# Optimization experiments

Hardware: AMD Instinct MI355X
Metric: run time of the kernel (lower is better)

## Reference

```python
import jax, jax.numpy as jnp
import numpy as np

N, H, W = 4, 96, 96
C, G, K = 128, 8, 3
GC = C // G          # group channels = 16
P = K * K            # sampling points per group = 9
PAD = K // 2
OFS = 1.0            # offset_scale
HID = 4 * C          # mlp hidden
EPS = 1e-5           # torch nn.LayerNorm default eps


def _ln(x, g, b):
    m = jnp.mean(x, -1, keepdims=True)
    v = jnp.mean((x - m) ** 2, -1, keepdims=True)
    return (x - m) * jax.lax.rsqrt(v + EPS) * g + b


def _dcnv3_core(x, offset, mask):
    # x: (n,H,W,C) channels-last, offset: (n,H,W,G*P*2), mask: (n,H,W,G,P) softmaxed.
    # Faithful port of dcnv3_core_pytorch (stride=1, dilation=1, zero-pad grid_sample,
    # align_corners=False -> pixel = loc*size - 0.5).
    n = x.shape[0]
    xp = jnp.pad(x, ((0, 0), (PAD, PAD), (PAD, PAD), (0, 0)))
    Hin, Win = H + 2 * PAD, W + 2 * PAD
    L = H * W
    base = (K - 1) // 2 + 0.5
    ref_x = (base + jnp.arange(W, dtype=x.dtype)) / Win  # normalized by padded size
    ref_y = (base + jnp.arange(H, dtype=x.dtype)) / Hin
    k = jnp.arange(K, dtype=x.dtype) - (K - 1) // 2
    dx = jnp.repeat(k, K) / Win  # torch meshgrid('ij'): kernel-x varies slowest
    dy = jnp.tile(k, K) / Hin
    off = offset.reshape(n, H, W, G, P, 2)
    # absolute sampling pixel coords (grid_sample align_corners=False)
    px = (ref_x[None, None, :, None, None] + dx * OFS + off[..., 0] * OFS / Win) * Win - 0.5
    py = (ref_y[None, :, None, None, None] + dy * OFS + off[..., 1] * OFS / Hin) * Hin - 0.5
    # layout (n,G,L,P)
    px = px.transpose(0, 3, 1, 2, 4).reshape(n, G, L, P)
    py = py.transpose(0, 3, 1, 2, 4).reshape(n, G, L, P)
    mk = mask.transpose(0, 3, 1, 2, 4).reshape(n, G, L, P)
    xg = xp.reshape(n, Hin * Win, G, GC).transpose(0, 2, 1, 3)
    x0 = jnp.floor(px); y0 = jnp.floor(py)
    fx = px - x0; fy = py - y0
    x0 = x0.astype(jnp.int32); y0 = y0.astype(jnp.int32)
    x1 = x0 + 1; y1 = y0 + 1
    out = jnp.zeros((n, G, L, GC), x.dtype)
    for yi, xi, w in ((y0, x0, (1 - fy) * (1 - fx)), (y0, x1, (1 - fy) * fx),
                      (y1, x0, fy * (1 - fx)), (y1, x1, fy * fx)):
        valid = (yi >= 0) & (yi < Hin) & (xi >= 0) & (xi < Win)
        idx = jnp.clip(yi, 0, Hin - 1) * Win + jnp.clip(xi, 0, Win - 1)
        v = jnp.take_along_axis(xg, idx.reshape(n, G, L * P, 1), axis=2)
        v = v.reshape(n, G, L, P, GC)
        out = out + jnp.einsum('nglp,nglpc->nglc', jnp.where(valid, w, 0.0) * mk, v)
    return out.transpose(0, 2, 1, 3).reshape(n, H, W, C)


def _dcn(x, w_in, b_in, dw_k, dw_b, dwg, dwb, w_off, b_off, w_msk, b_msk, w_out, b_out):
    n = x.shape[0]
    xproj = x @ w_in + b_in
    x1 = jax.lax.conv_general_dilated(
        x, dw_k, (1, 1), 'SAME',
        dimension_numbers=('NHWC', 'HWIO', 'NHWC'),
        feature_group_count=C) + dw_b
    x1 = jax.nn.gelu(_ln(x1, dwg, dwb), approximate=False)
    offset = x1 @ w_off + b_off
    mask = jax.nn.softmax((x1 @ w_msk + b_msk).reshape(n, H, W, G, P), axis=-1)
    y = _dcnv3_core(xproj, offset, mask)
    return y @ w_out + b_out


def setup_inputs() -> dict:
    key = jax.random.key(0)
    ks = jax.random.split(key, 10)
    rn = lambda k, s, sc: jax.random.normal(k, s, jnp.float32) * sc
    return {
        'x': rn(ks[0], (N, H, W, C), 1.0),
        'ln1g': jnp.ones((C,), jnp.float32), 'ln1b': jnp.zeros((C,), jnp.float32),
        'w_in': rn(ks[1], (C, C), 0.02), 'b_in': jnp.zeros((C,), jnp.float32),
        'dw_k': rn(ks[2], (K, K, 1, C), 0.1), 'dw_b': jnp.zeros((C,), jnp.float32),
        'dwg': jnp.ones((C,), jnp.float32), 'dwb': jnp.zeros((C,), jnp.float32),
        'w_off': rn(ks[3], (C, G * P * 2), 0.01), 'b_off': rn(ks[4], (G * P * 2,), 0.1),
        'w_msk': rn(ks[5], (C, G * P), 0.02), 'b_msk': jnp.zeros((G * P,), jnp.float32),
        'w_out': rn(ks[6], (C, C), 0.02), 'b_out': jnp.zeros((C,), jnp.float32),
        'ln2g': jnp.ones((C,), jnp.float32), 'ln2b': jnp.zeros((C,), jnp.float32),
        'w1': rn(ks[7], (C, HID), 0.02), 'b1': jnp.zeros((HID,), jnp.float32),
        'w2': rn(ks[8], (HID, C), 0.02), 'b2': jnp.zeros((C,), jnp.float32),
    }


def reference(x, ln1g, ln1b, w_in, b_in, dw_k, dw_b, dwg, dwb, w_off, b_off,
              w_msk, b_msk, w_out, b_out, ln2g, ln2b, w1, b1, w2, b2):
    # pre-norm InternImage block: x = x + dcn(LN1(x)); x = x + mlp(LN2(x))
    x = x + _dcn(_ln(x, ln1g, ln1b), w_in, b_in, dw_k, dw_b, dwg, dwb,
                 w_off, b_off, w_msk, b_msk, w_out, b_out)
    h = _ln(x, ln2g, ln2b)
    h = jax.nn.gelu(h @ w1 + b1, approximate=False) @ w2 + b2
    return x + h
```

## Files before the change

### kernel.cpp

```cpp
#include <hip/hip_runtime.h>
#include <hip/hip_bf16.h>
#include <math.h>

using bf16 = __hip_bfloat16;
using bf162 = __hip_bfloat162;

typedef __bf16 bf16x8 __attribute__((ext_vector_type(8)));
typedef float floatx4 __attribute__((ext_vector_type(4)));

constexpr int NB = 4, HH = 96, WW = 96, CC = 128, GG = 8, PP = 9;
constexpr int HW = HH * WW;
constexpr int NPIX = NB * HW;

__device__ __forceinline__ float ld1(const float* p) { return *p; }
__device__ __forceinline__ float ld1(const bf16* p)  { return __bfloat162float(*p); }
__device__ __forceinline__ void st1(float* p, float v) { *p = v; }
__device__ __forceinline__ void st1(bf16* p, float v)  { *p = __float2bfloat16(v); }
__device__ __forceinline__ float b2f(bf16 v) { return __bfloat162float(v); }
__device__ __forceinline__ bf16 f2b(float v) { return __float2bfloat16(v); }
__device__ __forceinline__ float gelu_exact(float v) {
    return 0.5f * v * (1.0f + erff(v * 0.7071067811865475f));
}
__device__ __forceinline__ floatx4 MFMA(bf16x8 a, bf16x8 b, floatx4 c) {
    return __builtin_amdgcn_mfma_f32_16x16x32_bf16(a, b, c, 0, 0, 0);
}

struct PrepArgs {
    const float* src[6];
    bf16* dst[6];
    int K[6], N[6];
    int cum[7];
    const float* b_off; const float* b_msk; float* b_om;
};

__global__ __launch_bounds__(256) void prep_weights(PrepArgs pa, int total)
{
    int t = blockIdx.x * 256 + threadIdx.x;
    if (t >= total) return;
    if (t >= pa.cum[6]) {
        int e = t - pa.cum[6];
        pa.b_om[e] = (e < 144) ? pa.b_off[e] : pa.b_msk[e - 144];
        return;
    }
    int i = 0;
    #pragma unroll
    for (int j = 0; j < 5; ++j) if (t >= pa.cum[j + 1]) i = j + 1;
    int e = t - pa.cum[i];
    int Ki = pa.K[i], Ni = pa.N[i];
    int n = e / Ki, k = e - n * Ki;
    pa.dst[i][e] = f2b(pa.src[i][(size_t)k * Ni + n]);
}

template<typename TI, typename TO>
__global__ __launch_bounds__(256) void ln_kernel(
    const TI* __restrict__ X, const float* __restrict__ g,
    const float* __restrict__ b, TO* __restrict__ out)
{
    int wave = (blockIdx.x * 256 + threadIdx.x) >> 6;
    int lane = threadIdx.x & 63;
    if (wave >= NPIX) return;
    const TI* xp = X + (size_t)wave * 128 + 2 * lane;
    float v0 = ld1(xp), v1 = ld1(xp + 1);
    float s = v0 + v1, q = v0 * v0 + v1 * v1;
    #pragma unroll
    for (int o = 32; o; o >>= 1) { s += __shfl_xor(s, o); q += __shfl_xor(q, o); }
    float mean = s * (1.0f / 128.0f);
    float rstd = rsqrtf(q * (1.0f / 128.0f) - mean * mean + 1e-5f);
    float g0 = g[2 * lane], g1 = g[2 * lane + 1];
    float b0 = b[2 * lane], b1 = b[2 * lane + 1];
    TO* op = out + (size_t)wave * 128 + 2 * lane;
    st1(op,     (v0 - mean) * rstd * g0 + b0);
    st1(op + 1, (v1 - mean) * rstd * g1 + b1);
}

__global__ __launch_bounds__(256) void dwconv_ln_gelu_kernel(
    const bf16* __restrict__ xln, const float* __restrict__ dwk,
    const float* __restrict__ dwb, const float* __restrict__ gam,
    const float* __restrict__ bet, bf16* __restrict__ out)
{
    int wave = (blockIdx.x * 256 + threadIdx.x) >> 6;
    int lane = threadIdx.x & 63;
    if (wave >= NPIX) return;
    int n = wave / HW; int rem = wave % HW;
    int y = rem / WW;  int x = rem % WW;
    const bf162* xp = (const bf162*)xln;
    float a0 = 0.f, a1 = 0.f;
    #pragma unroll
    for (int ky = 0; ky < 3; ++ky) {
        int yy = y + ky - 1;
        if (yy < 0 || yy >= HH) continue;
        #pragma unroll
        for (int kx = 0; kx < 3; ++kx) {
            int xx = x + kx - 1;
            if (xx < 0 || xx >= WW) continue;
            bf162 v = xp[((size_t)(n * HH + yy) * WW + xx) * 64 + lane];
            const float* w = dwk + (ky * 3 + kx) * CC + 2 * lane;
            a0 = fmaf(b2f(v.x), w[0], a0);
            a1 = fmaf(b2f(v.y), w[1], a1);
        }
    }
    a0 += dwb[2 * lane]; a1 += dwb[2 * lane + 1];
    float s = a0 + a1, q = a0 * a0 + a1 * a1;
    #pragma unroll
    for (int o = 32; o; o >>= 1) { s += __shfl_xor(s, o); q += __shfl_xor(q, o); }
    float mean = s * (1.0f / 128.0f);
    float rstd = rsqrtf(q * (1.0f / 128.0f) - mean * mean + 1e-5f);
    float h0 = gelu_exact((a0 - mean) * rstd * gam[2 * lane]     + bet[2 * lane]);
    float h1 = gelu_exact((a1 - mean) * rstd * gam[2 * lane + 1] + bet[2 * lane + 1]);
    bf162 o2; o2.x = f2b(h0); o2.y = f2b(h1);
    ((bf162*)out)[(size_t)wave * 64 + lane] = o2;
}

__global__ __launch_bounds__(256) void dcn_core_kernel(
    const bf16* __restrict__ xproj, const bf16* __restrict__ omr,
    bf16* __restrict__ out)
{
    __shared__ int4   sOff[4][72];
    __shared__ float4 sW[4][72];
    __shared__ float  sRaw[4][72];
    int wv = threadIdx.x >> 6;
    int lane = threadIdx.x & 63;
    int pix = blockIdx.x * 4 + wv;
    int n = pix / HW; int rem = pix % HW;
    int iy = rem / WW; int ix = rem % WW;
    const bf16* om = omr + (size_t)pix * 216;

    for (int e = lane; e < 72; e += 64)
        sRaw[wv][e] = b2f(om[144 + e]);
    __syncthreads();

    for (int e = lane; e < 72; e += 64) {
        int g = e / 9, p = e - 9 * g;
        float mx = -1e30f;
        #pragma unroll
        for (int i = 0; i < 9; ++i) mx = fmaxf(mx, sRaw[wv][g * 9 + i]);
        float ssum = 0.f;
        #pragma unroll
        for (int i = 0; i < 9; ++i) ssum += __expf(sRaw[wv][g * 9 + i] - mx);
        float mw = __expf(sRaw[wv][e] - mx) / ssum;

        float ox = b2f(om[g * 18 + 2 * p]);
        float oy = b2f(om[g * 18 + 2 * p + 1]);
        int kx = p / 3 - 1, ky = p % 3 - 1;
        float px = (float)(ix + kx) + ox;
        float py = (float)(iy + ky) + oy;
        float fx0 = floorf(px), fy0 = floorf(py);
        int x0 = (int)fx0, y0 = (int)fy0;
        float fx = px - fx0, fy = py - fy0;
        bool vx0 = (x0 >= 0) & (x0 < WW), vx1 = (x0 + 1 >= 0) & (x0 + 1 < WW);
        bool vy0 = (y0 >= 0) & (y0 < HH), vy1 = (y0 + 1 >= 0) & (y0 + 1 < HH);
        float w00 = (1.f - fy) * (1.f - fx) * mw * (vy0 && vx0 ? 1.f : 0.f);
        float w01 = (1.f - fy) * fx         * mw * (vy0 && vx1 ? 1.f : 0.f);
        float w10 = fy * (1.f - fx)         * mw * (vy1 && vx0 ? 1.f : 0.f);
        float w11 = fy * fx                 * mw * (vy1 && vx1 ? 1.f : 0.f);
        int x0c = min(max(x0, 0), WW - 1), x1c = min(max(x0 + 1, 0), WW - 1);
        int y0c = min(max(y0, 0), HH - 1), y1c = min(max(y0 + 1, 0), HH - 1);
        sOff[wv][e] = make_int4((y0c * WW + x0c) * CC, (y0c * WW + x1c) * CC,
                                (y1c * WW + x0c) * CC, (y1c * WW + x1c) * CC);
        sW[wv][e] = make_float4(w00, w01, w10, w11);
    }
    __syncthreads();

    const bf16* xb = xproj + (size_t)n * HW * CC + 2 * lane;
    int gbase = (lane >> 3) * 9;
    float a0 = 0.f, a1 = 0.f;
    #pragma unroll
    for (int p = 0; p < 9; ++p) {
        int4 o = sOff[wv][gbase + p];
        float4 w = sW[wv][gbase + p];
        bf162 v00 = *(const bf162*)(xb + o.x);
        bf162 v01 = *(const bf162*)(xb + o.y);
        bf162 v10 = *(const bf162*)(xb + o.z);
        bf162 v11 = *(const bf162*)(xb + o.w);
        a0 += w.x * b2f(v00.x) + w.y * b2f(v01.x) + w.z * b2f(v10.x) + w.w * b2f(v11.x);
        a1 += w.x * b2f(v00.y) + w.y * b2f(v01.y) + w.z * b2f(v10.y) + w.w * b2f(v11.y);
    }
    bf162 o2; o2.x = f2b(a0); o2.y = f2b(a1);
    ((bf162*)out)[(size_t)pix * 64 + lane] = o2;
}

__global__ __launch_bounds__(256) void gemm_mfma_kernel(
    const bf16* __restrict__ A, const bf16* __restrict__ Wt,
    const float* __restrict__ bias, bf16* __restrict__ Out, int M, int Nn, int K)
{
    __shared__ __align__(16) __bf16 As[64][72];
    __shared__ __align__(16) __bf16 Bs[64][72];
    int tid = threadIdx.x;
    int wv = tid >> 6, lane = tid & 63;
    int bm = blockIdx.y * 64, bn = blockIdx.x * 64;
    int mI = lane & 15, q = lane >> 4;
    floatx4 acc[4] = {};

    for (int k0 = 0; k0 < K; k0 += 64) {
        #pragma unroll
        for (int cc = 0; cc < 2; ++cc) {
            int ch = tid * 2 + cc;
            int row = ch >> 3, ko = (ch & 7) * 8;
            *reinterpret_cast<uint4*>(&As[row][ko]) =
                *reinterpret_cast<const uint4*>(A + (size_t)(bm + row) * K + k0 + ko);
            int ng = bn + row;
            uint4 bv = make_uint4(0, 0, 0, 0);
            if (ng < Nn) bv = *reinterpret_cast<const uint4*>(Wt + (size_t)ng * K + k0 + ko);
            *reinterpret_cast<uint4*>(&Bs[row][ko]) = bv;
        }
        __syncthreads();
        #pragma unroll
        for (int kk = 0; kk < 64; kk += 32) {
            bf16x8 a = *reinterpret_cast<const bf16x8*>(&As[wv * 16 + mI][kk + q * 8]);
            #pragma unroll
            for (int t = 0; t < 4; ++t) {
                bf16x8 b = *reinterpret_cast<const bf16x8*>(&Bs[t * 16 + mI][kk + q * 8]);
                acc[t] = MFMA(a, b, acc[t]);
            }
        }
        __syncthreads();
    }
    int row0 = bm + wv * 16 + q * 4;
    #pragma unroll
    for (int t = 0; t < 4; ++t) {
        int col = bn + t * 16 + mI;
        if (col >= Nn) continue;
        float bs = bias[col];
        #pragma unroll
        for (int r = 0; r < 4; ++r)
            st1(Out + (size_t)(row0 + r) * Nn + col, acc[t][r] + bs);
    }
}

__global__ __launch_bounds__(256, 2) void fused_tail_kernel(
    const bf16* __restrict__ ycore, const float* __restrict__ x,
    const bf16* __restrict__ w_outT, const float* __restrict__ b_out,
    const float* __restrict__ ln2g, const float* __restrict__ ln2b,
    const bf16* __restrict__ w1T, const float* __restrict__ b1,
    const bf16* __restrict__ w2T, const float* __restrict__ b2,
    float* __restrict__ out)
{
    __shared__ __align__(16) bf16 sU[64 * 264];
    __shared__ __align__(16) bf16 sXres[64 * 136];
    __shared__ __align__(16) bf16 sH2[64 * 136];
    int tid = threadIdx.x, wv = tid >> 6, lane = tid & 63;
    int mI = lane & 15, q = lane >> 4;
    int bm = blockIdx.x * 64;

    #pragma unroll
    for (int i = 0; i < 4; ++i) {
        int s = tid + 256 * i;
        int row = s >> 4, ko = (s & 15) * 8;
        *reinterpret_cast<uint4*>(&sU[row * 136 + ko]) =
            *reinterpret_cast<const uint4*>(ycore + (size_t)(bm + row) * 128 + ko);
    }
    __syncthreads();

    floatx4 acc0[4][2] = {};
    #pragma unroll
    for (int ks = 0; ks < 4; ++ks) {
        int k = ks * 32 + q * 8;
        bf16x8 a[4];
        #pragma unroll
        for (int rt = 0; rt < 4; ++rt)
            a[rt] = *reinterpret_cast<const bf16x8*>(&sU[(rt * 16 + mI) * 136 + k]);
        #pragma unroll
        for (int ct = 0; ct < 2; ++ct) {
            bf16x8 b = *reinterpret_cast<const bf16x8*>(
                w_outT + (size_t)(wv * 32 + ct * 16 + mI) * 128 + k);
            #pragma unroll
            for (int rt = 0; rt < 4; ++rt) acc0[rt][ct] = MFMA(a[rt], b, acc0[rt][ct]);
        }
    }
    #pragma unroll
    for (int rt = 0; rt < 4; ++rt)
        #pragma unroll
        for (int ct = 0; ct < 2; ++ct) {
            int col = wv * 32 + ct * 16 + mI;
            float bs = b_out[col];
            #pragma unroll
            for (int r = 0; r < 4; ++r) {
                int row = rt * 16 + q * 4 + r;
                float v = acc0[rt][ct][r] + bs + x[(size_t)(bm + row) * 128 + col];
                sXres[row * 136 + col] = f2b(v);
            }
        }
    __syncthreads();

    {
        int row = tid >> 2, part = tid & 3;
        float s = 0.f, sq = 0.f;
        float vals[32];
        #pragma unroll
        for (int j = 0; j < 4; ++j) {
            bf16x8 v = *reinterpret_cast<const bf16x8*>(&sXres[row * 136 + part * 32 + j * 8]);
            #pragma unroll
            for (int e = 0; e < 8; ++e) {
                float f = (float)v[e];
                vals[j * 8 + e] = f; s += f; sq += f * f;
            }
        }
        s  += __shfl_xor(s, 1);  s += __shfl_xor(s, 2);
        sq += __shfl_xor(sq, 1); sq += __shfl_xor(sq, 2);
        float mean = s * (1.0f / 128.0f);
        float rstd = rsqrtf(sq * (1.0f / 128.0f) - mean * mean + 1e-5f);
        #pragma unroll
        for (int j = 0; j < 4; ++j) {
            bf16x8 o;
            #pragma unroll
            for (int e = 0; e < 8; ++e) {
                int ch = part * 32 + j * 8 + e;
                bf16 t = f2b((vals[j * 8 + e] - mean) * rstd * ln2g[ch] + ln2b[ch]);
                o[e] = *reinterpret_cast<__bf16*>(&t);
            }
            *reinterpret_cast<bf16x8*>(&sH2[row * 136 + part * 32 + j * 8]) = o;
        }
    }
    __syncthreads();

    floatx4 acc2[4][2] = {};
    for (int h = 0; h < 2; ++h) {
        floatx4 acc1[4][4] = {};
        #pragma unroll
        for (int ks = 0; ks < 4; ++ks) {
            int k = ks * 32 + q * 8;
            bf16x8 a[4];
            #pragma unroll
            for (int rt = 0; rt < 4; ++rt)
                a[rt] = *reinterpret_cast<const bf16x8*>(&sH2[(rt * 16 + mI) * 136 + k]);
            #pragma unroll
            for (int ct = 0; ct < 4; ++ct) {
                int gcol = h * 256 + wv * 64 + ct * 16 + mI;
                bf16x8 b = *reinterpret_cast<const bf16x8*>(w1T + (size_t)gcol * 128 + k);
                #pragma unroll
                for (int rt = 0; rt < 4; ++rt) acc1[rt][ct] = MFMA(a[rt], b, acc1[rt][ct]);
            }
        }
        #pragma unroll
        for (int rt = 0; rt < 4; ++rt)
            #pragma unroll
            for (int ct = 0; ct < 4; ++ct) {
                int lcol = wv * 64 + ct * 16 + mI;
                float bs = b1[h * 256 + lcol];
                #pragma unroll
                for (int r = 0; r < 4; ++r) {
                    int row = rt * 16 + q * 4 + r;
                    sU[row * 264 + lcol] = f2b(gelu_exact(acc1[rt][ct][r] + bs));
                }
            }
        __syncthreads();
        #pragma unroll
        for (int ks = 0; ks < 8; ++ks) {
            int k = ks * 32 + q * 8;
            bf16x8 a[4];
            #pragma unroll
            for (int rt = 0; rt < 4; ++rt)
                a[rt] = *reinterpret_cast<const bf16x8*>(&sU[(rt * 16 + mI) * 264 + k]);
            #pragma unroll
            for (int ct = 0; ct < 2; ++ct) {
                int ng = wv * 32 + ct * 16 + mI;
                bf16x8 b = *reinterpret_cast<const bf16x8*>(
                    w2T + (size_t)ng * 512 + h * 256 + k);
                #pragma unroll
                for (int rt = 0; rt < 4; ++rt) acc2[rt][ct] = MFMA(a[rt], b, acc2[rt][ct]);
            }
        }
        __syncthreads();
    }
    #pragma unroll
    for (int rt = 0; rt < 4; ++rt)
        #pragma unroll
        for (int ct = 0; ct < 2; ++ct) {
            int col = wv * 32 + ct * 16 + mI;
            float bs = b2[col];
            #pragma unroll
            for (int r = 0; r < 4; ++r) {
                int row = rt * 16 + q * 4 + r;
                out[(size_t)(bm + row) * 128 + col] =
                    acc2[rt][ct][r] + bs + b2f(sXres[row * 136 + col]);
            }
        }
}

extern "C" void kernel_launch(void* const* d_in, const int* in_sizes, int n_in,
                              void* d_out, int out_size, void* d_ws, size_t ws_size,
                              hipStream_t stream)
{
    const float* x     = (const float*)d_in[0];
    const float* ln1g  = (const float*)d_in[1];
    const float* ln1b  = (const float*)d_in[2];
    const float* w_in  = (const float*)d_in[3];
    const float* b_in  = (const float*)d_in[4];
    const float* dw_k  = (const float*)d_in[5];
    const float* dw_b  = (const float*)d_in[6];
    const float* dwg   = (const float*)d_in[7];
    const float* dwb   = (const float*)d_in[8];
    const float* w_off = (const float*)d_in[9];
    const float* b_off = (const float*)d_in[10];
    const float* w_msk = (const float*)d_in[11];
    const float* b_msk = (const float*)d_in[12];
    const float* w_out = (const float*)d_in[13];
    const float* b_out = (const float*)d_in[14];
    const float* ln2g  = (const float*)d_in[15];
    const float* ln2b  = (const float*)d_in[16];
    const float* w1    = (const float*)d_in[17];
    const float* b1    = (const float*)d_in[18];
    const float* w2    = (const float*)d_in[19];
    const float* b2    = (const float*)d_in[20];
    float* out = (float*)d_out;

    bf16* ws = (bf16*)d_ws;
    bf16* xln   = ws;
    bf16* xproj = xln   + (size_t)NPIX * 128;
    bf16* x1    = xproj + (size_t)NPIX * 128;
    bf16* omr   = x1    + (size_t)NPIX * 128;
    bf16* ycore = xln;
    bf16* wT    = ws + (size_t)NPIX * 600;
    bf16* w_inT  = wT;
    bf16* w_omT  = w_inT  + 16384;
    bf16* w_outT = w_omT  + 27648;
    bf16* w1T    = w_outT + 16384;
    bf16* w2T    = w1T    + 65536;
    float* b_om  = (float*)(w2T + 65536);
    const int WTOT = 191488 + 216;

    PrepArgs pa;
    pa.src[0] = w_in;  pa.dst[0] = w_inT;            pa.K[0] = 128; pa.N[0] = 128;
    pa.src[1] = w_off; pa.dst[1] = w_omT;            pa.K[1] = 128; pa.N[1] = 144;
    pa.src[2] = w_msk; pa.dst[2] = w_omT + 144*128;  pa.K[2] = 128; pa.N[2] = 72;
    pa.src[3] = w_out; pa.dst[3] = w_outT;           pa.K[3] = 128; pa.N[3] = 128;
    pa.src[4] = w1;    pa.dst[4] = w1T;              pa.K[4] = 128; pa.N[4] = 512;
    pa.src[5] = w2;    pa.dst[5] = w2T;              pa.K[5] = 512; pa.N[5] = 128;
    pa.cum[0] = 0;     pa.cum[1] = 16384;  pa.cum[2] = 34816; pa.cum[3] = 44032;
    pa.cum[4] = 60416; pa.cum[5] = 125952; pa.cum[6] = 191488;
    pa.b_off = b_off;  pa.b_msk = b_msk;   pa.b_om = b_om;

    const int M = NPIX;
    dim3 blk(256);

    prep_weights<<<(WTOT + 255) / 256, blk, 0, stream>>>(pa, WTOT);
    ln_kernel<float, bf16><<<NPIX / 4, blk, 0, stream>>>(x, ln1g, ln1b, xln);
    gemm_mfma_kernel<<<dim3(2, M / 64), blk, 0, stream>>>(
        xln, w_inT, b_in, xproj, M, 128, 128);
    dwconv_ln_gelu_kernel<<<NPIX / 4, blk, 0, stream>>>(xln, dw_k, dw_b, dwg, dwb, x1);
    gemm_mfma_kernel<<<dim3(4, M / 64), blk, 0, stream>>>(
        x1, w_omT, b_om, omr, M, 216, 128);
    dcn_core_kernel<<<NPIX / 4, blk, 0, stream>>>(xproj, omr, ycore);
    fused_tail_kernel<<<M / 64, blk, 0, stream>>>(
        ycore, x, w_outT, b_out, ln2g, ln2b, w1T, b1, w2T, b2, out);
}
```

Baseline: 245.2 us.

## Split MLP hidden into quarter phases, prefetch weight fragments, shrink LDS for occupancy

```diff
diff --git a/kernel.cpp b/kernel.cpp
--- a/kernel.cpp
+++ b/kernel.cpp
@@ -227,7 +227,7 @@
     }
 }
 
-__global__ __launch_bounds__(256, 2) void fused_tail_kernel(
+__global__ __launch_bounds__(256, 3) void fused_tail_kernel(
     const bf16* __restrict__ ycore, const float* __restrict__ x,
     const bf16* __restrict__ w_outT, const float* __restrict__ b_out,
     const float* __restrict__ ln2g, const float* __restrict__ ln2b,
@@ -235,18 +235,26 @@
     const bf16* __restrict__ w2T, const float* __restrict__ b2,
     float* __restrict__ out)
 {
-    __shared__ __align__(16) bf16 sU[64 * 264];
+    __shared__ __align__(16) bf16 sA[64 * 136];
     __shared__ __align__(16) bf16 sXres[64 * 136];
     __shared__ __align__(16) bf16 sH2[64 * 136];
     int tid = threadIdx.x, wv = tid >> 6, lane = tid & 63;
     int mI = lane & 15, q = lane >> 4;
     int bm = blockIdx.x * 64;
 
+    bf16x8 bw0[4][2];
+    #pragma unroll
+    for (int ks = 0; ks < 4; ++ks)
+        #pragma unroll
+        for (int ct = 0; ct < 2; ++ct)
+            bw0[ks][ct] = *reinterpret_cast<const bf16x8*>(
+                w_outT + (size_t)(wv * 32 + ct * 16 + mI) * 128 + ks * 32 + q * 8);
+
     #pragma unroll
     for (int i = 0; i < 4; ++i) {
         int s = tid + 256 * i;
         int row = s >> 4, ko = (s & 15) * 8;
-        *reinterpret_cast<uint4*>(&sU[row * 136 + ko]) =
+        *reinterpret_cast<uint4*>(&sA[row * 136 + ko]) =
             *reinterpret_cast<const uint4*>(ycore + (size_t)(bm + row) * 128 + ko);
     }
     __syncthreads();
@@ -258,14 +266,12 @@
         bf16x8 a[4];
         #pragma unroll
         for (int rt = 0; rt < 4; ++rt)
-            a[rt] = *reinterpret_cast<const bf16x8*>(&sU[(rt * 16 + mI) * 136 + k]);
-        #pragma unroll
-        for (int ct = 0; ct < 2; ++ct) {
-            bf16x8 b = *reinterpret_cast<const bf16x8*>(
-                w_outT + (size_t)(wv * 32 + ct * 16 + mI) * 128 + k);
-            #pragma unroll
-            for (int rt = 0; rt < 4; ++rt) acc0[rt][ct] = MFMA(a[rt], b, acc0[rt][ct]);
-        }
+            a[rt] = *reinterpret_cast<const bf16x8*>(&sA[(rt * 16 + mI) * 136 + k]);
+        #pragma unroll
+        for (int ct = 0; ct < 2; ++ct)
+            #pragma unroll
+            for (int rt = 0; rt < 4; ++rt)
+                acc0[rt][ct] = MFMA(a[rt], bw0[ks][ct], acc0[rt][ct]);
     }
     #pragma unroll
     for (int rt = 0; rt < 4; ++rt)
@@ -314,8 +320,16 @@
     __syncthreads();
 
     floatx4 acc2[4][2] = {};
-    for (int h = 0; h < 2; ++h) {
-        floatx4 acc1[4][4] = {};
+    #pragma unroll 1
+    for (int ph = 0; ph < 4; ++ph) {
+        bf16x8 bw1[4][2];
+        #pragma unroll
+        for (int ks = 0; ks < 4; ++ks)
+            #pragma unroll
+            for (int ct = 0; ct < 2; ++ct)
+                bw1[ks][ct] = *reinterpret_cast<const bf16x8*>(
+                    w1T + (size_t)(ph * 128 + wv * 32 + ct * 16 + mI) * 128 + ks * 32 + q * 8);
+        floatx4 acc1[4][2] = {};
         #pragma unroll
         for (int ks = 0; ks < 4; ++ks) {
             int k = ks * 32 + q * 8;
@@ -324,43 +338,45 @@
             for (int rt = 0; rt < 4; ++rt)
                 a[rt] = *reinterpret_cast<const bf16x8*>(&sH2[(rt * 16 + mI) * 136 + k]);
             #pragma unroll
-            for (int ct = 0; ct < 4; ++ct) {
-                int gcol = h * 256 + wv * 64 + ct * 16 + mI;
-                bf16x8 b = *reinterpret_cast<const bf16x8*>(w1T + (size_t)gcol * 128 + k);
+            for (int ct = 0; ct < 2; ++ct)
                 #pragma unroll
-                for (int rt = 0; rt < 4; ++rt) acc1[rt][ct] = MFMA(a[rt], b, acc1[rt][ct]);
-            }
-        }
+                for (int rt = 0; rt < 4; ++rt)
+                    acc1[rt][ct] = MFMA(a[rt], bw1[ks][ct], acc1[rt][ct]);
+        }
+        __syncthreads();
+        bf16x8 bw2[4][2];
+        #pragma unroll
+        for (int ks = 0; ks < 4; ++ks)
+            #pragma unroll
+            for (int ct = 0; ct < 2; ++ct)
+                bw2[ks][ct] = *reinterpret_cast<const bf16x8*>(
+                    w2T + (size_t)(wv * 32 + ct * 16 + mI) * 512 + ph * 128 + ks * 32 + q * 8);
         #pragma unroll
         for (int rt = 0; rt < 4; ++rt)
             #pragma unroll
-            for (int ct = 0; ct < 4; ++ct) {
-                int lcol = wv * 64 + ct * 16 + mI;
-                float bs = b1[h * 256 + lcol];
+            for (int ct = 0; ct < 2; ++ct) {
+                int lcol = wv * 32 + ct * 16 + mI;
+                float bs = b1[ph * 128 + lcol];
                 #pragma unroll
                 for (int r = 0; r < 4; ++r) {
                     int row = rt * 16 + q * 4 + r;
-                    sU[row * 264 + lcol] = f2b(gelu_exact(acc1[rt][ct][r] + bs));
+                    sA[row * 136 + lcol] = f2b(gelu_exact(acc1[rt][ct][r] + bs));
                 }
             }
         __syncthreads();
         #pragma unroll
-        for (int ks = 0; ks < 8; ++ks) {
+        for (int ks = 0; ks < 4; ++ks) {
             int k = ks * 32 + q * 8;
             bf16x8 a[4];
             #pragma unroll
             for (int rt = 0; rt < 4; ++rt)
-                a[rt] = *reinterpret_cast<const bf16x8*>(&sU[(rt * 16 + mI) * 264 + k]);
-            #pragma unroll
-            for (int ct = 0; ct < 2; ++ct) {
-                int ng = wv * 32 + ct * 16 + mI;
-                bf16x8 b = *reinterpret_cast<const bf16x8*>(
-                    w2T + (size_t)ng * 512 + h * 256 + k);
+                a[rt] = *reinterpret_cast<const bf16x8*>(&sA[(rt * 16 + mI) * 136 + k]);
+            #pragma unroll
+            for (int ct = 0; ct < 2; ++ct)
                 #pragma unroll
-                for (int rt = 0; rt < 4; ++rt) acc2[rt][ct] = MFMA(a[rt], b, acc2[rt][ct]);
-            }
-        }
-        __syncthreads();
+                for (int rt = 0; rt < 4; ++rt)
+                    acc2[rt][ct] = MFMA(a[rt], bw2[ks][ct], acc2[rt][ct]);
+        }
     }
     #pragma unroll
     for (int rt = 0; rt < 4; ++rt)
```

New measurement: 236.9 us. -3.4%, faster.
